# Kernel optimization log

Measured on AMD Instinct MI355X. Metric: run time of the kernel, lower is better.

Reference implementation:

```python
import jax, jax.numpy as jnp
import numpy as np

NUM_ITER = 2
NUM_SLOTS = 3
D = 64          # slot_dim
MLP_H = 64
C_IN = 512
N = 262144      # number of input features (pixels)
EPS = 1e-8
LN_EPS = 1e-3   # keras LayerNormalization default


def _ln(x, g, b):
    m = jnp.mean(x, axis=-1, keepdims=True)
    v = jnp.var(x, axis=-1, keepdims=True)
    return (x - m) * jax.lax.rsqrt(v + LN_EPS) * g + b


def _gru(x, h, k, rk, bias):
    # keras GRUCell, reset_after=True; bias: [2, 3D] (input bias, recurrent bias)
    xm = x @ k + bias[0]
    hm = h @ rk + bias[1]
    xz, xr, xh = jnp.split(xm, 3, axis=-1)
    hz, hr, hh = jnp.split(hm, 3, axis=-1)
    z = jax.nn.sigmoid(xz + hz)
    r = jax.nn.sigmoid(xr + hr)
    cand = jnp.tanh(xh + r * hh)
    return z * h + (1.0 - z) * cand


def _mlp(s, g, b, W1, b1, W2, b2):
    h = _ln(s, g, b)
    return jax.nn.relu(h @ W1 + b1) @ W2 + b2


def _glorot(key, shape):
    fan_in, fan_out = shape[0], shape[-1]
    lim = np.sqrt(6.0 / (fan_in + fan_out))
    return jax.random.uniform(key, shape, jnp.float32, -lim, lim)


def setup_inputs() -> dict:
    key = jax.random.key(0)
    ks = jax.random.split(key, 24)
    inp = {
        'x': jax.random.normal(ks[0], (N, C_IN), jnp.float32),
        'noise_fg': jax.random.normal(ks[1], (NUM_SLOTS - 1, D), jnp.float32),
        'noise_bg': jax.random.normal(ks[2], (1, D), jnp.float32),
        'ln_g': jnp.ones((C_IN,), jnp.float32),
        'ln_b': jnp.zeros((C_IN,), jnp.float32),
        'mu_fg': _glorot(ks[3], (1, D)),
        'ls_fg': _glorot(ks[4], (1, D)),
        'mu_bg': _glorot(ks[5], (1, D)),
        'ls_bg': _glorot(ks[6], (1, D)),
        'Wk': _glorot(ks[7], (C_IN, D)),
        'Wv': _glorot(ks[8], (C_IN, D)),
        'qfg_g': jnp.ones((D,), jnp.float32), 'qfg_b': jnp.zeros((D,), jnp.float32),
        'qfg_W': _glorot(ks[9], (D, D)),
        'qbg_g': jnp.ones((D,), jnp.float32), 'qbg_b': jnp.zeros((D,), jnp.float32),
        'qbg_W': _glorot(ks[10], (D, D)),
        'grufg_k': _glorot(ks[11], (D, 3 * D)),
        'grufg_rk': _glorot(ks[12], (D, 3 * D)),
        'grufg_bias': jnp.zeros((2, 3 * D), jnp.float32),
        'grubg_k': _glorot(ks[13], (D, 3 * D)),
        'grubg_rk': _glorot(ks[14], (D, 3 * D)),
        'grubg_bias': jnp.zeros((2, 3 * D), jnp.float32),
        'mlpfg_g': jnp.ones((D,), jnp.float32), 'mlpfg_b': jnp.zeros((D,), jnp.float32),
        'mlpfg_W1': _glorot(ks[15], (D, MLP_H)), 'mlpfg_b1': jnp.zeros((MLP_H,), jnp.float32),
        'mlpfg_W2': _glorot(ks[16], (MLP_H, D)), 'mlpfg_b2': jnp.zeros((D,), jnp.float32),
        'mlpbg_g': jnp.ones((D,), jnp.float32), 'mlpbg_b': jnp.zeros((D,), jnp.float32),
        'mlpbg_W1': _glorot(ks[17], (D, MLP_H)), 'mlpbg_b1': jnp.zeros((MLP_H,), jnp.float32),
        'mlpbg_W2': _glorot(ks[18], (MLP_H, D)), 'mlpbg_b2': jnp.zeros((D,), jnp.float32),
    }
    return inp


def reference(x, noise_fg, noise_bg, ln_g, ln_b, mu_fg, ls_fg, mu_bg, ls_bg,
              Wk, Wv, qfg_g, qfg_b, qfg_W, qbg_g, qbg_b, qbg_W,
              grufg_k, grufg_rk, grufg_bias, grubg_k, grubg_rk, grubg_bias,
              mlpfg_g, mlpfg_b, mlpfg_W1, mlpfg_b1, mlpfg_W2, mlpfg_b2,
              mlpbg_g, mlpbg_b, mlpbg_W1, mlpbg_b1, mlpbg_W2, mlpbg_b2):
    x = _ln(x, ln_g, ln_b)
    slots_fg = mu_fg + jnp.exp(ls_fg) * noise_fg      # [K-1, D]
    slots_bg = mu_bg + jnp.exp(ls_bg) * noise_bg      # [1, D]
    k = x @ Wk                                        # [N, D]
    v = x @ Wv                                        # [N, D]
    scale = D ** (-0.5)
    attn = None
    for _ in range(NUM_ITER):
        q_fg = _ln(slots_fg, qfg_g, qfg_b) @ qfg_W * scale
        q_bg = _ln(slots_bg, qbg_g, qbg_b) @ qbg_W * scale
        logits = jnp.concatenate([k @ q_bg.T, k @ q_fg.T], axis=-1)  # [N, K]
        attn = jax.nn.softmax(logits, axis=-1)
        attn_bg, attn_fg = attn[:, 0:1], attn[:, 1:]
        w_bg = attn_bg + EPS
        w_bg = w_bg / jnp.sum(w_bg, axis=-2, keepdims=True)
        upd_bg = w_bg.T @ v                                          # [1, D]
        w_fg = attn_fg + EPS
        w_fg = w_fg / jnp.sum(w_fg, axis=-2, keepdims=True)
        upd_fg = w_fg.T @ v                                          # [K-1, D]
        slots_bg = _gru(upd_bg, slots_bg, grubg_k, grubg_rk, grubg_bias)
        slots_fg = _gru(upd_fg, slots_fg, grufg_k, grufg_rk, grufg_bias)
        slots_bg = slots_bg + _mlp(slots_bg, mlpbg_g, mlpbg_b, mlpbg_W1, mlpbg_b1, mlpbg_W2, mlpbg_b2)
        slots_fg = slots_fg + _mlp(slots_fg, mlpfg_g, mlpfg_b, mlpfg_W1, mlpfg_b1, mlpfg_W2, mlpfg_b2)
    slots = jnp.concatenate([slots_bg, slots_fg], axis=0)            # [K, D]
    return slots, attn.T                                             # [K,D], [K,N]
```

## Files before the change

### kernel.cpp

```cpp
#include <hip/hip_runtime.h>
#include <hip/hip_bf16.h>


#define N_TOK 262144
#define CIN 512
#define TILE_M 64
#define NBLK_A 512
#define NBLK_I2 1024
#define PSTRIDE 1024

typedef __attribute__((ext_vector_type(8))) short short8;
typedef __attribute__((ext_vector_type(4))) float f32x4;

__device__ __forceinline__ unsigned short f2bf(float f) {
    union { float f; unsigned u; } v; v.f = f;
    unsigned r = v.u + 0x7FFFu + ((v.u >> 16) & 1u);
    return (unsigned short)(r >> 16);
}
__device__ __forceinline__ unsigned pkbf(float a, float b) {
    return (unsigned)f2bf(a) | ((unsigned)f2bf(b) << 16);
}
__device__ __forceinline__ float bf2f(unsigned short u) {
    union { unsigned u; float f; } v; v.u = ((unsigned)u) << 16;
    return v.f;
}
__device__ __forceinline__ float sigmoidf_(float x) { return 1.f / (1.f + expf(-x)); }

__device__ __forceinline__ float q_from_slot(float v, const float* __restrict__ g,
                                             const float* __restrict__ b,
                                             const float* __restrict__ W, int lane) {
    float s = v, s2 = v * v;
#pragma unroll
    for (int d = 1; d < 64; d <<= 1) { s += __shfl_xor(s, d); s2 += __shfl_xor(s2, d); }
    float mean = s * (1.f / 64.f);
    float var = s2 * (1.f / 64.f) - mean * mean;
    float rstd = rsqrtf(var + 1e-3f);
    float hl = (v - mean) * rstd * g[lane] + b[lane];
    float acc = 0.f;
    for (int i = 0; i < 64; ++i) acc += __shfl(hl, i) * W[i * 64 + lane];
    return acc * 0.125f;
}

__global__ __launch_bounds__(256) void wt_init_kernel(
    const float* __restrict__ Wk, const float* __restrict__ Wv,
    const float* __restrict__ ln_g, const float* __restrict__ ln_b,
    unsigned short* __restrict__ Wt, float* __restrict__ c12,
    const float* __restrict__ noise_fg, const float* __restrict__ noise_bg,
    const float* __restrict__ mu_fg, const float* __restrict__ ls_fg,
    const float* __restrict__ mu_bg, const float* __restrict__ ls_bg,
    const float* __restrict__ qbg_g, const float* __restrict__ qbg_b, const float* __restrict__ qbg_W,
    const float* __restrict__ qfg_g, const float* __restrict__ qfg_b, const float* __restrict__ qfg_W,
    float* __restrict__ slots_ws, float* __restrict__ q_ws) {
    int t = threadIdx.x;
    if (blockIdx.x < 128) {
        int j = blockIdx.x;
        const float* W = (j < 64) ? Wk : Wv;
        int jc = j & 63;
        float c1 = 0.f, c2 = 0.f;
        for (int i = t; i < 512; i += 256) {
            float wv = W[i * 64 + jc];
            float g = ln_g[i], b = ln_b[i];
            c1 += g * wv; c2 += b * wv;
            Wt[(size_t)j * 512 + i] = f2bf(g * wv);
        }
        __shared__ float s1[4], s2[4];
#pragma unroll
        for (int d = 1; d < 64; d <<= 1) { c1 += __shfl_xor(c1, d); c2 += __shfl_xor(c2, d); }
        if ((t & 63) == 0) { s1[t >> 6] = c1; s2[t >> 6] = c2; }
        __syncthreads();
        if (t == 0) {
            c12[j] = (s1[0] + s1[1]) + (s1[2] + s1[3]);
            c12[128 + j] = (s2[0] + s2[1]) + (s2[2] + s2[3]);
        }
    } else {
        if (t < 192) {
            int s = t >> 6, c = t & 63;
            float v = (s == 0) ? (mu_bg[c] + expf(ls_bg[c]) * noise_bg[c])
                               : (mu_fg[c] + expf(ls_fg[c]) * noise_fg[(s - 1) * 64 + c]);
            slots_ws[t] = v;
            const float* g = s ? qfg_g : qbg_g;
            const float* b = s ? qfg_b : qbg_b;
            const float* W = s ? qfg_W : qbg_W;
            q_ws[t] = q_from_slot(v, g, b, W, c);
        }
    }
}

__global__ __launch_bounds__(256, 2) void phaseA_kernel(
    const float* __restrict__ x, const unsigned short* __restrict__ Wt,
    const float* __restrict__ c12, const float* __restrict__ qv,
    unsigned short* __restrict__ kb, unsigned short* __restrict__ vb,
    float* __restrict__ partials) {
    __shared__ unsigned short SA[TILE_M * CIN];
    __shared__ float q_s[192];
    __shared__ float w_s[64 * 4];
    __shared__ float2 rowstat[64];
    float* kvf = (float*)SA;

    const int t = threadIdx.x;
    const int lane = t & 63;
    const int w = t >> 6;

    if (t < 192) q_s[t] = qv[t];

    short8 bfrag[16][2];
    float c1r[2], c2r[2];
#pragma unroll
    for (int nt = 0; nt < 2; ++nt) {
        int col = w * 32 + nt * 16 + (lane & 15);
        c1r[nt] = c12[col];
        c2r[nt] = c12[128 + col];
#pragma unroll
        for (int kk = 0; kk < 16; ++kk) {
            int off = kk * 32 + ((lane >> 4) << 3);
            bfrag[kk][nt] = *(const short8*)(Wt + (size_t)col * 512 + off);
        }
    }

    float upd_acc = 0.f;
    float sw_acc = 0.f;

    for (int tile = blockIdx.x; tile < N_TOK / TILE_M; tile += NBLK_A) {
        const size_t row0 = (size_t)tile * TILE_M;
        __syncthreads();

#pragma unroll
        for (int p = 0; p < 2; ++p) {
            int r = w * 16 + p * 8 + (lane >> 3);
            int c8 = lane & 7;
            const float4* xr = (const float4*)(x + (row0 + r) * CIN) + c8 * 16;
            char* rowbase = (char*)SA + r * 1024;
            int bb = c8 * 128;
            int sw = (r & 7) << 4;
            float s = 0.f, s2 = 0.f;
#pragma unroll
            for (int i = 0; i < 8; ++i) {
                float4 a = xr[2 * i];
                float4 b = xr[2 * i + 1];
                s += (a.x + a.y) + (a.z + a.w) + (b.x + b.y) + (b.z + b.w);
                s2 = fmaf(a.x, a.x, s2); s2 = fmaf(a.y, a.y, s2);
                s2 = fmaf(a.z, a.z, s2); s2 = fmaf(a.w, a.w, s2);
                s2 = fmaf(b.x, b.x, s2); s2 = fmaf(b.y, b.y, s2);
                s2 = fmaf(b.z, b.z, s2); s2 = fmaf(b.w, b.w, s2);
                uint4 o;
                o.x = pkbf(a.x, a.y); o.y = pkbf(a.z, a.w);
                o.z = pkbf(b.x, b.y); o.w = pkbf(b.z, b.w);
                *(uint4*)(rowbase + ((bb + i * 16) ^ sw)) = o;
            }
#pragma unroll
            for (int d = 1; d < 8; d <<= 1) { s += __shfl_xor(s, d); s2 += __shfl_xor(s2, d); }
            if (c8 == 0) {
                float mean = s * (1.f / 512.f);
                float var = s2 * (1.f / 512.f) - mean * mean;
                float rstd = rsqrtf(var + 1e-3f);
                rowstat[r] = make_float2(rstd, mean * rstd);
            }
        }
        __syncthreads();

        f32x4 acc[4][2];
#pragma unroll
        for (int m = 0; m < 4; ++m) {
            acc[m][0] = (f32x4){0.f, 0.f, 0.f, 0.f};
            acc[m][1] = (f32x4){0.f, 0.f, 0.f, 0.f};
        }
#pragma unroll
        for (int kk = 0; kk < 16; ++kk) {
#pragma unroll
            for (int m = 0; m < 4; ++m) {
                int row = m * 16 + (lane & 15);
                int boff = (kk * 64 + ((lane >> 4) << 4)) ^ ((row & 7) << 4);
                short8 af = *(const short8*)((const char*)SA + row * 1024 + boff);
                acc[m][0] = __builtin_amdgcn_mfma_f32_16x16x32_bf16(af, bfrag[kk][0], acc[m][0], 0, 0, 0);
                acc[m][1] = __builtin_amdgcn_mfma_f32_16x16x32_bf16(af, bfrag[kk][1], acc[m][1], 0, 0, 0);
            }
        }
        __syncthreads();

        float2 rs[16];
#pragma unroll
        for (int m = 0; m < 4; ++m)
#pragma unroll
            for (int j = 0; j < 4; ++j)
                rs[m * 4 + j] = rowstat[m * 16 + ((lane >> 4) << 2) + j];
#pragma unroll
        for (int m = 0; m < 4; ++m)
#pragma unroll
            for (int n = 0; n < 2; ++n)
#pragma unroll
                for (int j = 0; j < 4; ++j) {
                    int row = m * 16 + ((lane >> 4) << 2) + j;
                    int col = w * 32 + n * 16 + (lane & 15);
                    float val = fmaf(rs[m * 4 + j].x, acc[m][n][j],
                                     fmaf(-rs[m * 4 + j].y, c1r[n], c2r[n]));
                    kvf[row * 130 + col] = val;
                }
        __syncthreads();

        {
            int r = t >> 2, q4 = t & 3;
            unsigned short* dst = ((q4 < 2) ? kb : vb) + (row0 + r) * 64 + (q4 & 1) * 32;
            const float* src = &kvf[r * 130 + q4 * 32];
#pragma unroll
            for (int j = 0; j < 32; j += 8) {
                float2 p0 = *(const float2*)(src + j);
                float2 p1 = *(const float2*)(src + j + 2);
                float2 p2 = *(const float2*)(src + j + 4);
                float2 p3 = *(const float2*)(src + j + 6);
                uint4 o;
                o.x = pkbf(p0.x, p0.y);
                o.y = pkbf(p1.x, p1.y);
                o.z = pkbf(p2.x, p2.y);
                o.w = pkbf(p3.x, p3.y);
                *(uint4*)(dst + j) = o;
            }
        }
        if (t < 64) {
            int r = t;
            float l0 = 0.f, l1 = 0.f, l2 = 0.f;
#pragma unroll 8
            for (int c = 0; c < 64; c += 2) {
                float2 kv2 = *(const float2*)&kvf[r * 130 + c];
                l0 += kv2.x * q_s[c] + kv2.y * q_s[c + 1];
                l1 += kv2.x * q_s[64 + c] + kv2.y * q_s[64 + c + 1];
                l2 += kv2.x * q_s[128 + c] + kv2.y * q_s[128 + c + 1];
            }
            float mx = fmaxf(l0, fmaxf(l1, l2));
            float e0 = expf(l0 - mx), e1 = expf(l1 - mx), e2 = expf(l2 - mx);
            float inv = 1.f / (e0 + e1 + e2);
            w_s[r * 4 + 0] = e0 * inv + 1e-8f;
            w_s[r * 4 + 1] = e1 * inv + 1e-8f;
            w_s[r * 4 + 2] = e2 * inv + 1e-8f;
        }
        __syncthreads();

        if (t < 192) {
            int s = t >> 6, c = t & 63;
            float a = 0.f;
            for (int r = 0; r < 64; ++r) a += w_s[r * 4 + s] * kvf[r * 130 + 64 + c];
            upd_acc += a;
        } else if (t < 195) {
            int s = t - 192;
            float a = 0.f;
            for (int r = 0; r < 64; ++r) a += w_s[r * 4 + s];
            sw_acc += a;
        }
    }
    if (t < 192) partials[(size_t)t * PSTRIDE + blockIdx.x] = upd_acc;
    else if (t < 195) partials[(size_t)t * PSTRIDE + blockIdx.x] = sw_acc;
}

__global__ __launch_bounds__(256) void iter2_kernel(
    const unsigned short* __restrict__ kb, const unsigned short* __restrict__ vb,
    const float* __restrict__ qv, float* __restrict__ attn_out, float* __restrict__ partials) {
    __shared__ float q_s[192];
    __shared__ float w_s[256 * 4];
    __shared__ unsigned short v_lds[256 * 64];
    int t = threadIdx.x;
    if (t < 192) q_s[t] = qv[t];
    __syncthreads();
    size_t r = (size_t)blockIdx.x * 256 + t;
    const unsigned short* krow = kb + r * 64;
    float l0 = 0.f, l1 = 0.f, l2 = 0.f;
#pragma unroll
    for (int i = 0; i < 8; ++i) {
        uint4 u = *(const uint4*)(krow + i * 8);
        unsigned uu[4] = {u.x, u.y, u.z, u.w};
#pragma unroll
        for (int p = 0; p < 4; ++p) {
            float fa = bf2f((unsigned short)(uu[p] & 0xffffu));
            float fb = bf2f((unsigned short)(uu[p] >> 16));
            int c = i * 8 + p * 2;
            l0 += fa * q_s[c] + fb * q_s[c + 1];
            l1 += fa * q_s[64 + c] + fb * q_s[64 + c + 1];
            l2 += fa * q_s[128 + c] + fb * q_s[128 + c + 1];
        }
    }
    float mx = fmaxf(l0, fmaxf(l1, l2));
    float e0 = expf(l0 - mx), e1 = expf(l1 - mx), e2 = expf(l2 - mx);
    float inv = 1.f / (e0 + e1 + e2);
    float a0 = e0 * inv, a1 = e1 * inv, a2 = e2 * inv;
    attn_out[r] = a0;
    attn_out[(size_t)N_TOK + r] = a1;
    attn_out[2 * (size_t)N_TOK + r] = a2;
    w_s[t * 4 + 0] = a0 + 1e-8f;
    w_s[t * 4 + 1] = a1 + 1e-8f;
    w_s[t * 4 + 2] = a2 + 1e-8f;
    {
        const uint4* vr = (const uint4*)(vb + r * 64);
        uint4* vl = (uint4*)(v_lds + t * 64);
#pragma unroll
        for (int i = 0; i < 8; ++i) vl[i] = vr[i];
    }
    __syncthreads();
    if (t < 192) {
        int s = t >> 6, c = t & 63;
        float part = 0.f;
        for (int r2 = 0; r2 < 256; ++r2) part += w_s[r2 * 4 + s] * bf2f(v_lds[r2 * 64 + c]);
        partials[(size_t)t * PSTRIDE + blockIdx.x] = part;
    } else if (t < 195) {
        int s = t - 192;
        float part = 0.f;
        for (int r2 = 0; r2 < 256; ++r2) part += w_s[r2 * 4 + s];
        partials[(size_t)t * PSTRIDE + blockIdx.x] = part;
    }
}

__global__ __launch_bounds__(256) void reduce_kernel(const float* __restrict__ partials,
                                                     int nblk, float* __restrict__ reduced) {
    int col = blockIdx.x, t = threadIdx.x;
    float a = 0.f;
    for (int b = t; b < nblk; b += 256) a += partials[(size_t)col * PSTRIDE + b];
#pragma unroll
    for (int d = 1; d < 64; d <<= 1) a += __shfl_xor(a, d);
    __shared__ float ws_[4];
    if ((t & 63) == 0) ws_[t >> 6] = a;
    __syncthreads();
    if (t == 0) reduced[col] = (ws_[0] + ws_[1]) + (ws_[2] + ws_[3]);
}

__global__ __launch_bounds__(256) void update_kernel(
    const float* __restrict__ reduced,
    float* __restrict__ slots_ws, float* __restrict__ q_ws,
    const float* __restrict__ gbg_k, const float* __restrict__ gbg_rk, const float* __restrict__ gbg_bias,
    const float* __restrict__ gfg_k, const float* __restrict__ gfg_rk, const float* __restrict__ gfg_bias,
    const float* __restrict__ mbg_g, const float* __restrict__ mbg_b, const float* __restrict__ mbg_W1,
    const float* __restrict__ mbg_b1, const float* __restrict__ mbg_W2, const float* __restrict__ mbg_b2,
    const float* __restrict__ mfg_g, const float* __restrict__ mfg_b, const float* __restrict__ mfg_W1,
    const float* __restrict__ mfg_b1, const float* __restrict__ mfg_W2, const float* __restrict__ mfg_b2,
    const float* __restrict__ qbg_g, const float* __restrict__ qbg_b, const float* __restrict__ qbg_W,
    const float* __restrict__ qfg_g, const float* __restrict__ qfg_b, const float* __restrict__ qfg_W,
    int compute_q, float* __restrict__ out_slots) {
    __shared__ float upd[192], hslots[192], swv[3];
    __shared__ float xm[192], hm[192], gout[64], lnv[64], hid[64];
    int t = threadIdx.x;
    if (t < 192) { hslots[t] = slots_ws[t]; upd[t] = reduced[t]; }
    else if (t < 195) swv[t - 192] = reduced[t];
    __syncthreads();
    if (t < 192) upd[t] = upd[t] / swv[t >> 6];
    __syncthreads();

    for (int s = 0; s < 3; ++s) {
        const float* K = s ? gfg_k : gbg_k;
        const float* RK = s ? gfg_rk : gbg_rk;
        const float* BS = s ? gfg_bias : gbg_bias;
        if (t < 192) {
            float ax = BS[t], ah = BS[192 + t];
            const float* us = upd + s * 64;
            const float* hs = hslots + s * 64;
            for (int i = 0; i < 64; ++i) {
                ax += us[i] * K[i * 192 + t];
                ah += hs[i] * RK[i * 192 + t];
            }
            xm[t] = ax; hm[t] = ah;
        }
        __syncthreads();
        if (t < 64) {
            float z = sigmoidf_(xm[t] + hm[t]);
            float rg = sigmoidf_(xm[64 + t] + hm[64 + t]);
            float cand = tanhf(xm[128 + t] + rg * hm[128 + t]);
            gout[t] = z * hslots[s * 64 + t] + (1.f - z) * cand;
        }
        __syncthreads();
        const float* MG = s ? mfg_g : mbg_g;
        const float* MB = s ? mfg_b : mbg_b;
        const float* MW1 = s ? mfg_W1 : mbg_W1;
        const float* MB1 = s ? mfg_b1 : mbg_b1;
        const float* MW2 = s ? mfg_W2 : mbg_W2;
        const float* MB2 = s ? mfg_b2 : mbg_b2;
        if (t < 64) {
            float v = gout[t];
            float su = v, sq = v * v;
#pragma unroll
            for (int d = 1; d < 64; d <<= 1) { su += __shfl_xor(su, d); sq += __shfl_xor(sq, d); }
            float mean = su * (1.f / 64.f), var = sq * (1.f / 64.f) - mean * mean;
            float rstd = rsqrtf(var + 1e-3f);
            lnv[t] = (v - mean) * rstd * MG[t] + MB[t];
        }
        __syncthreads();
        if (t < 64) {
            float a = MB1[t];
            for (int i = 0; i < 64; ++i) a += lnv[i] * MW1[i * 64 + t];
            hid[t] = fmaxf(a, 0.f);
        }
        __syncthreads();
        if (t < 64) {
            float a = MB2[t];
            for (int i = 0; i < 64; ++i) a += hid[i] * MW2[i * 64 + t];
            hslots[s * 64 + t] = gout[t] + a;
        }
        __syncthreads();
    }
    if (t < 192) {
        slots_ws[t] = hslots[t];
        if (out_slots) out_slots[t] = hslots[t];
        if (compute_q) {
            int s = t >> 6, lane = t & 63;
            const float* g = s ? qfg_g : qbg_g;
            const float* b = s ? qfg_b : qbg_b;
            const float* W = s ? qfg_W : qbg_W;
            q_ws[t] = q_from_slot(hslots[t], g, b, W, lane);
        }
    }
}

extern "C" void kernel_launch(void* const* d_in, const int* in_sizes, int n_in,
                              void* d_out, int out_size, void* d_ws, size_t ws_size,
                              hipStream_t stream) {
    const float* x        = (const float*)d_in[0];
    const float* noise_fg = (const float*)d_in[1];
    const float* noise_bg = (const float*)d_in[2];
    const float* ln_g     = (const float*)d_in[3];
    const float* ln_b     = (const float*)d_in[4];
    const float* mu_fg    = (const float*)d_in[5];
    const float* ls_fg    = (const float*)d_in[6];
    const float* mu_bg    = (const float*)d_in[7];
    const float* ls_bg    = (const float*)d_in[8];
    const float* Wk       = (const float*)d_in[9];
    const float* Wv       = (const float*)d_in[10];
    const float* qfg_g    = (const float*)d_in[11];
    const float* qfg_b    = (const float*)d_in[12];
    const float* qfg_W    = (const float*)d_in[13];
    const float* qbg_g    = (const float*)d_in[14];
    const float* qbg_b    = (const float*)d_in[15];
    const float* qbg_W    = (const float*)d_in[16];
    const float* gfg_k    = (const float*)d_in[17];
    const float* gfg_rk   = (const float*)d_in[18];
    const float* gfg_bias = (const float*)d_in[19];
    const float* gbg_k    = (const float*)d_in[20];
    const float* gbg_rk   = (const float*)d_in[21];
    const float* gbg_bias = (const float*)d_in[22];
    const float* mfg_g    = (const float*)d_in[23];
    const float* mfg_b    = (const float*)d_in[24];
    const float* mfg_W1   = (const float*)d_in[25];
    const float* mfg_b1   = (const float*)d_in[26];
    const float* mfg_W2   = (const float*)d_in[27];
    const float* mfg_b2   = (const float*)d_in[28];
    const float* mbg_g    = (const float*)d_in[29];
    const float* mbg_b    = (const float*)d_in[30];
    const float* mbg_W1   = (const float*)d_in[31];
    const float* mbg_b1   = (const float*)d_in[32];
    const float* mbg_W2   = (const float*)d_in[33];
    const float* mbg_b2   = (const float*)d_in[34];

    char* ws = (char*)d_ws;
    unsigned short* Wt = (unsigned short*)ws;
    float* c12 = (float*)(ws + 131072);
    unsigned short* kb = (unsigned short*)(ws + 132096);
    unsigned short* vb = kb + (size_t)N_TOK * 64;
    char* ws2 = ws + 132096 + (size_t)2 * N_TOK * 64 * 2;
    float* slots_ws = (float*)ws2;
    float* q_ws = slots_ws + 192;
    float* reduced = q_ws + 192;
    float* partials = reduced + 256;

    float* out = (float*)d_out;

    wt_init_kernel<<<dim3(129), dim3(256), 0, stream>>>(
        Wk, Wv, ln_g, ln_b, Wt, c12,
        noise_fg, noise_bg, mu_fg, ls_fg, mu_bg, ls_bg,
        qbg_g, qbg_b, qbg_W, qfg_g, qfg_b, qfg_W, slots_ws, q_ws);
    phaseA_kernel<<<dim3(NBLK_A), dim3(256), 0, stream>>>(x, Wt, c12, q_ws, kb, vb, partials);
    reduce_kernel<<<dim3(195), dim3(256), 0, stream>>>(partials, NBLK_A, reduced);
    update_kernel<<<dim3(1), dim3(256), 0, stream>>>(reduced, slots_ws, q_ws,
        gbg_k, gbg_rk, gbg_bias, gfg_k, gfg_rk, gfg_bias,
        mbg_g, mbg_b, mbg_W1, mbg_b1, mbg_W2, mbg_b2,
        mfg_g, mfg_b, mfg_W1, mfg_b1, mfg_W2, mfg_b2,
        qbg_g, qbg_b, qbg_W, qfg_g, qfg_b, qfg_W, 1, (float*)nullptr);
    iter2_kernel<<<dim3(NBLK_I2), dim3(256), 0, stream>>>(kb, vb, q_ws, out + 192, partials);
    reduce_kernel<<<dim3(195), dim3(256), 0, stream>>>(partials, NBLK_I2, reduced);
    update_kernel<<<dim3(1), dim3(256), 0, stream>>>(reduced, slots_ws, q_ws,
        gbg_k, gbg_rk, gbg_bias, gfg_k, gfg_rk, gfg_bias,
        mbg_g, mbg_b, mbg_W1, mbg_b1, mbg_W2, mbg_b2,
        mfg_g, mfg_b, mfg_W1, mfg_b1, mfg_W2, mfg_b2,
        qbg_g, qbg_b, qbg_W, qfg_g, qfg_b, qfg_W, 0, out);
}
```

Baseline: 240.4 us.

## Warp-specialize phaseA into producer and MFMA consumer waves with double-buffered LDS

Phase A now runs 512-thread blocks where four waves load and convert the next x tile into a second LDS buffer while the other four waves run the MFMA projection, softmax and update accumulation on the current tile. The aim is to hide the global-memory load of x behind compute instead of serializing load and compute. The softmax and weighted-sum step is also spread across all consumer waves using shuffles, and partials are written per wave, so the reduce kernel sums four times as many entries. Occupancy drops to one block of 512 threads with about 130KB of LDS, and the grid is halved to 256 blocks, which may limit latency hiding.

```diff
diff --git a/kernel.cpp b/kernel.cpp
--- a/kernel.cpp
+++ b/kernel.cpp
@@ -5,7 +5,8 @@
 #define N_TOK 262144
 #define CIN 512
 #define TILE_M 64
-#define NBLK_A 512
+#define NT (N_TOK / TILE_M)
+#define NBLK_A 256
 #define NBLK_I2 1024
 #define PSTRIDE 1024
 
@@ -86,65 +87,60 @@
     }
 }
 
-__global__ __launch_bounds__(256, 2) void phaseA_kernel(
+__global__ __launch_bounds__(512, 1) void phaseA_kernel(
     const float* __restrict__ x, const unsigned short* __restrict__ Wt,
     const float* __restrict__ c12, const float* __restrict__ qv,
     unsigned short* __restrict__ kb, unsigned short* __restrict__ vb,
     float* __restrict__ partials) {
-    __shared__ unsigned short SA[TILE_M * CIN];
+    __shared__ unsigned short BUF[2][TILE_M * CIN];
     __shared__ float q_s[192];
-    __shared__ float w_s[64 * 4];
-    __shared__ float2 rowstat[64];
-    float* kvf = (float*)SA;
+    __shared__ float2 rowstat[2][TILE_M];
 
     const int t = threadIdx.x;
     const int lane = t & 63;
     const int w = t >> 6;
+    const bool is_prod = (w < 4);
+    const int vw = w & 3;
 
     if (t < 192) q_s[t] = qv[t];
 
     short8 bfrag[16][2];
     float c1r[2], c2r[2];
-#pragma unroll
-    for (int nt = 0; nt < 2; ++nt) {
-        int col = w * 32 + nt * 16 + (lane & 15);
-        c1r[nt] = c12[col];
-        c2r[nt] = c12[128 + col];
-#pragma unroll
-        for (int kk = 0; kk < 16; ++kk) {
-            int off = kk * 32 + ((lane >> 4) << 3);
-            bfrag[kk][nt] = *(const short8*)(Wt + (size_t)col * 512 + off);
-        }
-    }
-
-    float upd_acc = 0.f;
-    float sw_acc = 0.f;
-
-    for (int tile = blockIdx.x; tile < N_TOK / TILE_M; tile += NBLK_A) {
-        const size_t row0 = (size_t)tile * TILE_M;
-        __syncthreads();
-
+    float u0 = 0.f, u1 = 0.f, u2 = 0.f, sw0 = 0.f, sw1 = 0.f, sw2 = 0.f;
+    if (!is_prod) {
+#pragma unroll
+        for (int nt = 0; nt < 2; ++nt) {
+            int col = vw * 32 + nt * 16 + (lane & 15);
+            c1r[nt] = c12[col];
+            c2r[nt] = c12[128 + col];
+#pragma unroll
+            for (int kk = 0; kk < 16; ++kk)
+                bfrag[kk][nt] = *(const short8*)(Wt + (size_t)col * 512 + kk * 32 + ((lane >> 4) << 3));
+        }
+    }
+
+    auto produce = [&](int tile, int b) {
 #pragma unroll
         for (int p = 0; p < 2; ++p) {
-            int r = w * 16 + p * 8 + (lane >> 3);
+            int r = vw * 16 + p * 8 + (lane >> 3);
             int c8 = lane & 7;
-            const float4* xr = (const float4*)(x + (row0 + r) * CIN) + c8 * 16;
-            char* rowbase = (char*)SA + r * 1024;
+            const float4* xr = (const float4*)(x + ((size_t)tile * TILE_M + r) * CIN) + c8 * 16;
+            char* rowbase = (char*)&BUF[b][0] + r * 1024;
             int bb = c8 * 128;
             int sw = (r & 7) << 4;
             float s = 0.f, s2 = 0.f;
 #pragma unroll
             for (int i = 0; i < 8; ++i) {
                 float4 a = xr[2 * i];
-                float4 b = xr[2 * i + 1];
-                s += (a.x + a.y) + (a.z + a.w) + (b.x + b.y) + (b.z + b.w);
+                float4 bq = xr[2 * i + 1];
+                s += (a.x + a.y) + (a.z + a.w) + (bq.x + bq.y) + (bq.z + bq.w);
                 s2 = fmaf(a.x, a.x, s2); s2 = fmaf(a.y, a.y, s2);
                 s2 = fmaf(a.z, a.z, s2); s2 = fmaf(a.w, a.w, s2);
-                s2 = fmaf(b.x, b.x, s2); s2 = fmaf(b.y, b.y, s2);
-                s2 = fmaf(b.z, b.z, s2); s2 = fmaf(b.w, b.w, s2);
+                s2 = fmaf(bq.x, bq.x, s2); s2 = fmaf(bq.y, bq.y, s2);
+                s2 = fmaf(bq.z, bq.z, s2); s2 = fmaf(bq.w, bq.w, s2);
                 uint4 o;
                 o.x = pkbf(a.x, a.y); o.y = pkbf(a.z, a.w);
-                o.z = pkbf(b.x, b.y); o.w = pkbf(b.z, b.w);
+                o.z = pkbf(bq.x, bq.y); o.w = pkbf(bq.z, bq.w);
                 *(uint4*)(rowbase + ((bb + i * 16) ^ sw)) = o;
             }
 #pragma unroll
@@ -153,101 +149,138 @@
                 float mean = s * (1.f / 512.f);
                 float var = s2 * (1.f / 512.f) - mean * mean;
                 float rstd = rsqrtf(var + 1e-3f);
-                rowstat[r] = make_float2(rstd, mean * rstd);
-            }
-        }
-        __syncthreads();
+                rowstat[b][r] = make_float2(rstd, mean * rstd);
+            }
+        }
+    };
+
+    if (is_prod) produce(blockIdx.x, 0);
+    asm volatile("s_waitcnt vmcnt(0) lgkmcnt(0)" ::: "memory");
+    __builtin_amdgcn_s_barrier();
+
+    int cur = 0;
+    for (int tile = blockIdx.x; tile < NT; tile += NBLK_A) {
+        const size_t row0 = (size_t)tile * TILE_M;
+        const int nxt = tile + NBLK_A;
+        float* kvf = (float*)&BUF[cur][0];
 
         f32x4 acc[4][2];
-#pragma unroll
-        for (int m = 0; m < 4; ++m) {
-            acc[m][0] = (f32x4){0.f, 0.f, 0.f, 0.f};
-            acc[m][1] = (f32x4){0.f, 0.f, 0.f, 0.f};
-        }
-#pragma unroll
-        for (int kk = 0; kk < 16; ++kk) {
+        if (is_prod) {
+            if (nxt < NT) produce(nxt, cur ^ 1);
+        } else {
 #pragma unroll
             for (int m = 0; m < 4; ++m) {
-                int row = m * 16 + (lane & 15);
-                int boff = (kk * 64 + ((lane >> 4) << 4)) ^ ((row & 7) << 4);
-                short8 af = *(const short8*)((const char*)SA + row * 1024 + boff);
-                acc[m][0] = __builtin_amdgcn_mfma_f32_16x16x32_bf16(af, bfrag[kk][0], acc[m][0], 0, 0, 0);
-                acc[m][1] = __builtin_amdgcn_mfma_f32_16x16x32_bf16(af, bfrag[kk][1], acc[m][1], 0, 0, 0);
-            }
-        }
-        __syncthreads();
-
-        float2 rs[16];
-#pragma unroll
-        for (int m = 0; m < 4; ++m)
-#pragma unroll
-            for (int j = 0; j < 4; ++j)
-                rs[m * 4 + j] = rowstat[m * 16 + ((lane >> 4) << 2) + j];
-#pragma unroll
-        for (int m = 0; m < 4; ++m)
-#pragma unroll
-            for (int n = 0; n < 2; ++n)
+                acc[m][0] = (f32x4){0.f, 0.f, 0.f, 0.f};
+                acc[m][1] = (f32x4){0.f, 0.f, 0.f, 0.f};
+            }
+#pragma unroll
+            for (int kk = 0; kk < 16; ++kk) {
+#pragma unroll
+                for (int m = 0; m < 4; ++m) {
+                    int row = m * 16 + (lane & 15);
+                    int boff = (kk * 64 + ((lane >> 4) << 4)) ^ ((row & 7) << 4);
+                    short8 af = *(const short8*)((const char*)&BUF[cur][0] + row * 1024 + boff);
+                    acc[m][0] = __builtin_amdgcn_mfma_f32_16x16x32_bf16(af, bfrag[kk][0], acc[m][0], 0, 0, 0);
+                    acc[m][1] = __builtin_amdgcn_mfma_f32_16x16x32_bf16(af, bfrag[kk][1], acc[m][1], 0, 0, 0);
+                }
+            }
+#pragma unroll
+            for (int m = 0; m < 4; ++m)
 #pragma unroll
                 for (int j = 0; j < 4; ++j) {
-                    int row = m * 16 + ((lane >> 4) << 2) + j;
-                    int col = w * 32 + n * 16 + (lane & 15);
-                    float val = fmaf(rs[m * 4 + j].x, acc[m][n][j],
-                                     fmaf(-rs[m * 4 + j].y, c1r[n], c2r[n]));
-                    kvf[row * 130 + col] = val;
+                    float2 rs = rowstat[cur][m * 16 + ((lane >> 4) << 2) + j];
+#pragma unroll
+                    for (int n = 0; n < 2; ++n)
+                        acc[m][n][j] = fmaf(rs.x, acc[m][n][j], fmaf(-rs.y, c1r[n], c2r[n]));
                 }
-        __syncthreads();
-
-        {
-            int r = t >> 2, q4 = t & 3;
-            unsigned short* dst = ((q4 < 2) ? kb : vb) + (row0 + r) * 64 + (q4 & 1) * 32;
-            const float* src = &kvf[r * 130 + q4 * 32];
-#pragma unroll
-            for (int j = 0; j < 32; j += 8) {
-                float2 p0 = *(const float2*)(src + j);
-                float2 p1 = *(const float2*)(src + j + 2);
-                float2 p2 = *(const float2*)(src + j + 4);
-                float2 p3 = *(const float2*)(src + j + 6);
-                uint4 o;
-                o.x = pkbf(p0.x, p0.y);
-                o.y = pkbf(p1.x, p1.y);
-                o.z = pkbf(p2.x, p2.y);
-                o.w = pkbf(p3.x, p3.y);
-                *(uint4*)(dst + j) = o;
-            }
-        }
-        if (t < 64) {
-            int r = t;
-            float l0 = 0.f, l1 = 0.f, l2 = 0.f;
-#pragma unroll 8
-            for (int c = 0; c < 64; c += 2) {
-                float2 kv2 = *(const float2*)&kvf[r * 130 + c];
-                l0 += kv2.x * q_s[c] + kv2.y * q_s[c + 1];
-                l1 += kv2.x * q_s[64 + c] + kv2.y * q_s[64 + c + 1];
-                l2 += kv2.x * q_s[128 + c] + kv2.y * q_s[128 + c + 1];
-            }
-            float mx = fmaxf(l0, fmaxf(l1, l2));
-            float e0 = expf(l0 - mx), e1 = expf(l1 - mx), e2 = expf(l2 - mx);
-            float inv = 1.f / (e0 + e1 + e2);
-            w_s[r * 4 + 0] = e0 * inv + 1e-8f;
-            w_s[r * 4 + 1] = e1 * inv + 1e-8f;
-            w_s[r * 4 + 2] = e2 * inv + 1e-8f;
-        }
-        __syncthreads();
-
-        if (t < 192) {
-            int s = t >> 6, c = t & 63;
-            float a = 0.f;
-            for (int r = 0; r < 64; ++r) a += w_s[r * 4 + s] * kvf[r * 130 + 64 + c];
-            upd_acc += a;
-        } else if (t < 195) {
-            int s = t - 192;
-            float a = 0.f;
-            for (int r = 0; r < 64; ++r) a += w_s[r * 4 + s];
-            sw_acc += a;
-        }
-    }
-    if (t < 192) partials[(size_t)t * PSTRIDE + blockIdx.x] = upd_acc;
-    else if (t < 195) partials[(size_t)t * PSTRIDE + blockIdx.x] = sw_acc;
+        }
+        asm volatile("s_waitcnt lgkmcnt(0)" ::: "memory");
+        __builtin_amdgcn_s_barrier();
+
+        if (!is_prod) {
+#pragma unroll
+            for (int m = 0; m < 4; ++m)
+#pragma unroll
+                for (int n = 0; n < 2; ++n)
+#pragma unroll
+                    for (int j = 0; j < 4; ++j) {
+                        int row = m * 16 + ((lane >> 4) << 2) + j;
+                        int col = vw * 32 + n * 16 + (lane & 15);
+                        kvf[row * 130 + col] = acc[m][n][j];
+                    }
+        }
+        asm volatile("s_waitcnt lgkmcnt(0)" ::: "memory");
+        __builtin_amdgcn_s_barrier();
+
+        if (!is_prod) {
+            {
+                int ct = t - 256;
+                int r = ct >> 2, q4 = ct & 3;
+                unsigned short* dst = ((q4 < 2) ? kb : vb) + (row0 + r) * 64 + (q4 & 1) * 32;
+                const float* src = &kvf[r * 130 + q4 * 32];
+#pragma unroll
+                for (int j = 0; j < 32; j += 8) {
+                    float2 p0 = *(const float2*)(src + j);
+                    float2 p1 = *(const float2*)(src + j + 2);
+                    float2 p2 = *(const float2*)(src + j + 4);
+                    float2 p3 = *(const float2*)(src + j + 6);
+                    uint4 o;
+                    o.x = pkbf(p0.x, p0.y);
+                    o.y = pkbf(p1.x, p1.y);
+                    o.z = pkbf(p2.x, p2.y);
+                    o.w = pkbf(p3.x, p3.y);
+                    *(uint4*)(dst + j) = o;
+                }
+            }
+            {
+                int rr0 = vw * 16;
+                int cbase = (lane & 3) * 16;
+                float l0 = 0.f, l1 = 0.f, l2 = 0.f;
+                const float* kr = &kvf[(rr0 + (lane >> 2)) * 130 + cbase];
+#pragma unroll
+                for (int i = 0; i < 8; ++i) {
+                    float2 kv2 = *(const float2*)(kr + 2 * i);
+                    l0 += kv2.x * q_s[cbase + 2 * i] + kv2.y * q_s[cbase + 2 * i + 1];
+                    l1 += kv2.x * q_s[64 + cbase + 2 * i] + kv2.y * q_s[64 + cbase + 2 * i + 1];
+                    l2 += kv2.x * q_s[128 + cbase + 2 * i] + kv2.y * q_s[128 + cbase + 2 * i + 1];
+                }
+#pragma unroll
+                for (int d = 1; d < 4; d <<= 1) {
+                    l0 += __shfl_xor(l0, d); l1 += __shfl_xor(l1, d); l2 += __shfl_xor(l2, d);
+                }
+                float mx = fmaxf(l0, fmaxf(l1, l2));
+                float e0 = expf(l0 - mx), e1 = expf(l1 - mx), e2 = expf(l2 - mx);
+                float inv = 1.f / (e0 + e1 + e2);
+                float w0v = e0 * inv + 1e-8f;
+                float w1v = e1 * inv + 1e-8f;
+                float w2v = e2 * inv + 1e-8f;
+#pragma unroll
+                for (int rr = 0; rr < 16; ++rr) {
+                    float b0 = __shfl(w0v, rr * 4);
+                    float b1 = __shfl(w1v, rr * 4);
+                    float b2 = __shfl(w2v, rr * 4);
+                    float vv = kvf[(rr0 + rr) * 130 + 64 + lane];
+                    u0 = fmaf(b0, vv, u0); u1 = fmaf(b1, vv, u1); u2 = fmaf(b2, vv, u2);
+                    sw0 += b0; sw1 += b1; sw2 += b2;
+                }
+            }
+        }
+        asm volatile("s_waitcnt lgkmcnt(0)" ::: "memory");
+        __builtin_amdgcn_s_barrier();
+        cur ^= 1;
+    }
+
+    if (!is_prod) {
+        int slot = blockIdx.x * 4 + vw;
+        partials[(size_t)lane * PSTRIDE + slot] = u0;
+        partials[(size_t)(64 + lane) * PSTRIDE + slot] = u1;
+        partials[(size_t)(128 + lane) * PSTRIDE + slot] = u2;
+        if (lane == 0) {
+            partials[(size_t)192 * PSTRIDE + slot] = sw0;
+            partials[(size_t)193 * PSTRIDE + slot] = sw1;
+            partials[(size_t)194 * PSTRIDE + slot] = sw2;
+        }
+    }
 }
 
 __global__ __launch_bounds__(256) void iter2_kernel(
@@ -460,8 +493,8 @@
         Wk, Wv, ln_g, ln_b, Wt, c12,
         noise_fg, noise_bg, mu_fg, ls_fg, mu_bg, ls_bg,
         qbg_g, qbg_b, qbg_W, qfg_g, qfg_b, qfg_W, slots_ws, q_ws);
-    phaseA_kernel<<<dim3(NBLK_A), dim3(256), 0, stream>>>(x, Wt, c12, q_ws, kb, vb, partials);
-    reduce_kernel<<<dim3(195), dim3(256), 0, stream>>>(partials, NBLK_A, reduced);
+    phaseA_kernel<<<dim3(NBLK_A), dim3(512), 0, stream>>>(x, Wt, c12, q_ws, kb, vb, partials);
+    reduce_kernel<<<dim3(195), dim3(256), 0, stream>>>(partials, NBLK_A * 4, reduced);
     update_kernel<<<dim3(1), dim3(256), 0, stream>>>(reduced, slots_ws, q_ws,
         gbg_k, gbg_rk, gbg_bias, gfg_k, gfg_rk, gfg_bias,
         mbg_g, mbg_b, mbg_W1, mbg_b1, mbg_W2, mbg_b2,
```

Result: slower. 279.4 us (+16.2%).
